# Kernel tuning notes

Measured on AMD Instinct MI355X. Metric: run time of the kernel, lower is better.

The kernel has to match this reference:

```python
import jax, jax.numpy as jnp
import numpy as np
import math

WIN = (2, 7, 7)      # (wd, wh, ww) 3D window
SHIFT = (1, 3, 3)    # cyclic shift per dim
HEADS = 4
DIM = 128
MLP_HIDDEN = 4 * DIM


def _layernorm(x, w, b, eps=1e-5):
    m = x.mean(-1, keepdims=True)
    v = jnp.var(x, axis=-1, keepdims=True)
    return (x - m) * jax.lax.rsqrt(v + eps) * w + b


def setup_inputs() -> dict:
    key = jax.random.key(0)
    ks = jax.random.split(key, 6)
    C, H = DIM, MLP_HIDDEN
    p = lambda k, shape: jax.random.normal(k, shape, jnp.float32) * 0.02
    return {
        "x": jax.random.normal(ks[0], (4, 8, 56, 56, C), jnp.float32),
        "norm1_w": jnp.ones((C,), jnp.float32),
        "norm1_b": jnp.zeros((C,), jnp.float32),
        "qkv_w": p(ks[1], (C, 3 * C)),
        "qkv_b": jnp.zeros((3 * C,), jnp.float32),
        "proj_w": p(ks[2], (C, C)),
        "proj_b": jnp.zeros((C,), jnp.float32),
        "norm2_w": jnp.ones((C,), jnp.float32),
        "norm2_b": jnp.zeros((C,), jnp.float32),
        "fc1_w": p(ks[3], (C, H)),
        "fc1_b": jnp.zeros((H,), jnp.float32),
        "fc2_w": p(ks[4], (H, C)),
        "fc2_b": jnp.zeros((C,), jnp.float32),
    }


def reference(x, norm1_w, norm1_b, qkv_w, qkv_b, proj_w, proj_b,
              norm2_w, norm2_b, fc1_w, fc1_b, fc2_w, fc2_b):
    B, D, H, W, C = x.shape
    wd, wh, ww = WIN
    sd, sh, sw = SHIFT
    nd, nh, nw = D // wd, H // wh, W // ww
    N = wd * wh * ww          # tokens per window (98)
    hd = C // HEADS
    scale = 1.0 / math.sqrt(hd)

    # ---- part1: norm1 -> cyclic shift -> window partition -> MHA -> reverse ----
    h = _layernorm(x, norm1_w, norm1_b)
    h = jnp.roll(h, (-sd, -sh, -sw), axis=(1, 2, 3))
    # window partition: (B,D,H,W,C) -> (B*nWindows, N, C)
    xw = h.reshape(B, nd, wd, nh, wh, nw, ww, C)
    xw = xw.transpose(0, 1, 3, 5, 2, 4, 6, 7).reshape(-1, N, C)

    qkv = (xw @ qkv_w + qkv_b).reshape(-1, N, 3, HEADS, hd).transpose(2, 0, 3, 1, 4)
    q, k, v = qkv[0], qkv[1], qkv[2]      # each (Bw, heads, N, hd)
    scores = jnp.einsum('bhnc,bhmc->bhnm', q, k) * scale
    attn = jax.nn.softmax(scores, axis=-1)
    out = jnp.einsum('bhnm,bhmc->bhnc', attn, v)
    out = out.transpose(0, 2, 1, 3).reshape(-1, N, C)
    out = out @ proj_w + proj_b

    # window reverse: (B*nWindows, N, C) -> (B,D,H,W,C)
    out = out.reshape(B, nd, nh, nw, wd, wh, ww, C)
    out = out.transpose(0, 1, 4, 2, 5, 3, 6, 7).reshape(B, D, H, W, C)
    out = jnp.roll(out, (sd, sh, sw), axis=(1, 2, 3))

    x = x + out  # residual (drop_path = identity)

    # ---- part2: norm2 -> MLP (Linear -> SiLU -> Linear) -> residual ----
    h2 = _layernorm(x, norm2_w, norm2_b)
    h2 = jax.nn.silu(h2 @ fc1_w + fc1_b) @ fc2_w + fc2_b
    return x + h2
```

## Files before the change

### kernel.cpp

```cpp
#include <hip/hip_runtime.h>

typedef unsigned short u16;
typedef unsigned int u32;
typedef __bf16 bf16x8 __attribute__((ext_vector_type(8)));
typedef float f32x4 __attribute__((ext_vector_type(4)));
typedef u16 u16x8 __attribute__((ext_vector_type(8)));
typedef u16 u16x2 __attribute__((ext_vector_type(2)));

__device__ __forceinline__ float bf2f(u16 u) {
    union { u32 u; float f; } c; c.u = ((u32)u) << 16; return c.f;
}
__device__ __forceinline__ u16 f2bf(float f) {
    union { float f; u32 u; } c; c.f = f;
    u32 r = c.u + 0x7fffu + ((c.u >> 16) & 1u);
    return (u16)(r >> 16);
}
__device__ __forceinline__ u16 f2bfn(float f) {
    union { __bf16 h; u16 u; } c; c.h = (__bf16)f; return c.u;
}
__device__ __forceinline__ bf16x8 ld_frag(const u16* p) {
    return *reinterpret_cast<const bf16x8*>(p);
}

__global__ __launch_bounds__(256) void k_wT(
    const float* __restrict__ qkv_w, const float* __restrict__ proj_w,
    const float* __restrict__ fc1_w, const float* __restrict__ fc2_w,
    u16* __restrict__ qkvT, u16* __restrict__ projT,
    u16* __restrict__ fc1T, u16* __restrict__ fc2T)
{
    int t = blockIdx.x * 256 + threadIdx.x;
    if (t < 49152) { int k = t / 384, n = t % 384; qkvT[n*128 + k] = f2bf(qkv_w[t]); }
    if (t < 16384) { int k = t / 128, n = t % 128; projT[n*128 + k] = f2bf(proj_w[t]); }
    if (t < 65536) { int k = t / 512, n = t % 512; fc1T[n*128 + k] = f2bf(fc1_w[t]); }
    if (t < 65536) { int k = t / 128, n = t % 128; fc2T[n*512 + k] = f2bf(fc2_w[t]); }
}

__global__ __launch_bounds__(256) void k_ln1_part(
    const float* __restrict__ x, const float* __restrict__ w, const float* __restrict__ b,
    u16* __restrict__ xw)
{
    int wv = threadIdx.x >> 6, l = threadIdx.x & 63;
    int g = blockIdx.x * 4 + wv;
    int wi = g / 98, n = g % 98;
    int iw = wi & 7, ih = (wi >> 3) & 7, id = (wi >> 6) & 3, bb = wi >> 8;
    int tw = n % 7, tt = n / 7, th = tt % 7, td = tt / 7;
    int d  = (id * 2 + td + 1) & 7;
    int hh = ih * 7 + th + 3; if (hh >= 56) hh -= 56;
    int ww = iw * 7 + tw + 3; if (ww >= 56) ww -= 56;
    long src = ((((long)bb * 8 + d) * 56 + hh) * 56 + ww) * 128;
    float2 v = *(const float2*)(x + src + l * 2);
    float f0 = v.x, f1 = v.y;
    float s = f0 + f1, s2 = f0*f0 + f1*f1;
    #pragma unroll
    for (int o = 32; o; o >>= 1) { s += __shfl_xor(s, o); s2 += __shfl_xor(s2, o); }
    float mean = s * (1.f/128.f);
    float var  = s2 * (1.f/128.f) - mean*mean;
    float rstd = rsqrtf(var + 1e-5f);
    float y0 = (f0 - mean) * rstd * w[l*2]   + b[l*2];
    float y1 = (f1 - mean) * rstd * w[l*2+1] + b[l*2+1];
    u16x2 o2; o2[0] = f2bf(y0); o2[1] = f2bf(y1);
    *(u16x2*)(xw + (long)g * 128 + l * 2) = o2;
}

__global__ __launch_bounds__(256) void k_gemm128(
    const u16* __restrict__ A, const u16* __restrict__ BT,
    const float* __restrict__ bias, u16* __restrict__ out, int ldo)
{
    __shared__ __align__(16) u16 la[128*136];
    __shared__ __align__(16) u16 lb[128*136];
    int m0 = blockIdx.x * 128, n0 = blockIdx.y * 128;
    int t = threadIdx.x;
    #pragma unroll
    for (int i = 0; i < 8; i++) {
        int u = t + i * 256;
        int r = u >> 4, c = u & 15;
        *(u16x8*)&la[r*136 + c*8] = *(const u16x8*)&A [(long)(m0 + r)*128 + c*8];
        *(u16x8*)&lb[r*136 + c*8] = *(const u16x8*)&BT[(long)(n0 + r)*128 + c*8];
    }
    __syncthreads();
    int wv = t >> 6, l = t & 63;
    int wm = (wv & 1) * 64, wn = (wv >> 1) * 64;
    int lr = l & 15, lk = (l >> 4) * 8;
    f32x4 acc[4][4] = {};
    #pragma unroll
    for (int kk = 0; kk < 4; kk++) {
        bf16x8 af[4], bfr[4];
        #pragma unroll
        for (int mi = 0; mi < 4; mi++) af[mi]  = ld_frag(&la[(wm + mi*16 + lr)*136 + kk*32 + lk]);
        #pragma unroll
        for (int ni = 0; ni < 4; ni++) bfr[ni] = ld_frag(&lb[(wn + ni*16 + lr)*136 + kk*32 + lk]);
        #pragma unroll
        for (int mi = 0; mi < 4; mi++)
            #pragma unroll
            for (int ni = 0; ni < 4; ni++)
                acc[mi][ni] = __builtin_amdgcn_mfma_f32_16x16x32_bf16(af[mi], bfr[ni], acc[mi][ni], 0, 0, 0);
    }
    int rb = (l >> 4) * 4;
    #pragma unroll
    for (int mi = 0; mi < 4; mi++)
        #pragma unroll
        for (int ni = 0; ni < 4; ni++) {
            int col = n0 + wn + ni*16 + lr;
            float bv = bias[col];
            #pragma unroll
            for (int r = 0; r < 4; r++) {
                int row = m0 + wm + mi*16 + rb + r;
                out[(long)row*ldo + col] = f2bf(acc[mi][ni][r] + bv);
            }
        }
}

__global__ __launch_bounds__(256) void k_attn(
    const u16* __restrict__ qkv, u16* __restrict__ attn_out)
{
    __shared__ __align__(16) u16 lq[128*40];
    __shared__ __align__(16) u16 lk[128*40];
    __shared__ __align__(16) u16 lvt[32*136];
    __shared__ __align__(16) u16 lp[4][16*136];
    int wi = blockIdx.x, h = blockIdx.y;
    int t = threadIdx.x;
    int wv = t >> 6, l = t & 63;
    const long base = (long)wi * 98 * 384 + h * 32;
    u16* lpw = lp[wv];
    {
        u16x8 z8 = {};
        for (int i = l; i < 272; i += 64) *(u16x8*)&lpw[i*8] = z8;
    }
    #pragma unroll
    for (int i = 0; i < 4; i++) {
        int u = t + i * 256;
        int mat = u >> 9, row = (u >> 2) & 127, ch = u & 3;
        u16x8 v = {};
        if (row < 98) v = *(const u16x8*)&qkv[base + (long)row*384 + mat*128 + ch*8];
        u16* dst = mat ? lk : lq;
        *(u16x8*)&dst[row*40 + ch*8] = v;
    }
    #pragma unroll
    for (int i = 0; i < 2; i++) {
        int u = t + i * 256;
        int row = u >> 2, ch = u & 3;
        u16x8 v = {};
        if (row < 98) v = *(const u16x8*)&qkv[base + (long)row*384 + 256 + ch*8];
        #pragma unroll
        for (int j = 0; j < 8; j++) lvt[(ch*8 + j)*136 + row] = v[j];
    }
    __syncthreads();
    int lr = l & 15, lg = l >> 4, lkk = lg * 8;
    const float scale = 0.17677669529663687f;
    for (int rt = wv; rt < 7; rt += 4) {
        bf16x8 qa = ld_frag(&lq[(rt*16 + lr)*40 + lkk]);
        f32x4 s[7];
        #pragma unroll
        for (int ct = 0; ct < 7; ct++) {
            bf16x8 kb = ld_frag(&lk[(ct*16 + lr)*40 + lkk]);
            f32x4 zz = {0.f, 0.f, 0.f, 0.f};
            s[ct] = __builtin_amdgcn_mfma_f32_16x16x32_bf16(qa, kb, zz, 0, 0, 0);
        }
        #pragma unroll
        for (int ct = 0; ct < 7; ct++) {
            bool valid = (ct < 6) || (lr < 2);
            #pragma unroll
            for (int r = 0; r < 4; r++)
                s[ct][r] = valid ? s[ct][r] * scale : -1e30f;
        }
        f32x4 mx;
        #pragma unroll
        for (int r = 0; r < 4; r++) {
            float m = s[0][r];
            #pragma unroll
            for (int ct = 1; ct < 7; ct++) m = fmaxf(m, s[ct][r]);
            #pragma unroll
            for (int o = 1; o < 16; o <<= 1) m = fmaxf(m, __shfl_xor(m, o));
            mx[r] = m;
        }
        f32x4 sum = {0.f, 0.f, 0.f, 0.f};
        #pragma unroll
        for (int ct = 0; ct < 7; ct++)
            #pragma unroll
            for (int r = 0; r < 4; r++) {
                s[ct][r] = __expf(s[ct][r] - mx[r]);
                sum[r] += s[ct][r];
            }
        #pragma unroll
        for (int r = 0; r < 4; r++) {
            float ss = sum[r];
            #pragma unroll
            for (int o = 1; o < 16; o <<= 1) ss += __shfl_xor(ss, o);
            sum[r] = 1.f / ss;
        }
        #pragma unroll
        for (int ct = 0; ct < 7; ct++)
            #pragma unroll
            for (int r = 0; r < 4; r++)
                lpw[(lg*4 + r)*136 + ct*16 + lr] = f2bf(s[ct][r] * sum[r]);
        #pragma unroll
        for (int ni = 0; ni < 2; ni++) {
            f32x4 acc = {0.f, 0.f, 0.f, 0.f};
            #pragma unroll
            for (int kk = 0; kk < 4; kk++) {
                bf16x8 pa = ld_frag(&lpw[lr*136 + kk*32 + lkk]);
                bf16x8 vb = ld_frag(&lvt[(ni*16 + lr)*136 + kk*32 + lkk]);
                acc = __builtin_amdgcn_mfma_f32_16x16x32_bf16(pa, vb, acc, 0, 0, 0);
            }
            #pragma unroll
            for (int r = 0; r < 4; r++) {
                int row = rt*16 + lg*4 + r;
                if (row < 98)
                    attn_out[((long)wi*98 + row)*128 + h*32 + ni*16 + lr] = f2bf(acc[r]);
            }
        }
    }
}

__global__ __launch_bounds__(256, 4) void k_mlp2(
    const u16* __restrict__ pout, const float* __restrict__ x,
    const float* __restrict__ w2, const float* __restrict__ b2n,
    const u16* __restrict__ fc1T, const float* __restrict__ b1,
    const u16* __restrict__ fc2T, const float* __restrict__ b2,
    u16* __restrict__ x1g, float* __restrict__ out)
{
    __shared__ __align__(16) u16 lh [64*136];
    __shared__ __align__(16) u16 lhc[2][64*72];
    int m0 = blockIdx.x * 64;
    int t = threadIdx.x;
    int wv = t >> 6, l = t & 63;
    int lr = l & 15, lg = l >> 4, lk = lg * 8;
    {
        float4 w2a = *(const float4*)&w2 [lr*8];
        float4 w2b = *(const float4*)&w2 [lr*8 + 4];
        float4 b2a = *(const float4*)&b2n[lr*8];
        float4 b2b = *(const float4*)&b2n[lr*8 + 4];
        float w2v[8] = {w2a.x,w2a.y,w2a.z,w2a.w,w2b.x,w2b.y,w2b.z,w2b.w};
        float b2v[8] = {b2a.x,b2a.y,b2a.z,b2a.w,b2b.x,b2b.y,b2b.z,b2b.w};
        for (int it = 0; it < 4; it++) {
            int row = wv*16 + it*4 + lg;
            int g = m0 + row;
            int ww = g % 56; int t1 = g / 56;
            int hh = t1 % 56; int t2 = t1 / 56;
            int d = t2 & 7, bb = t2 >> 3;
            int d2 = (d + 7) & 7;
            int hs = hh - 3; if (hs < 0) hs += 56;
            int ws_ = ww - 3; if (ws_ < 0) ws_ += 56;
            int id = d2 >> 1, td = d2 & 1;
            int ih = hs / 7, th = hs % 7;
            int iw = ws_ / 7, tw = ws_ % 7;
            int wi = ((bb*4 + id)*8 + ih)*8 + iw;
            int n  = (td*7 + th)*7 + tw;
            long prow = ((long)wi*98 + n) * 128;
            u16x8 pv = *(const u16x8*)&pout[prow + lr*8];
            float4 xa = *(const float4*)&x[(long)g*128 + lr*8];
            float4 xb = *(const float4*)&x[(long)g*128 + lr*8 + 4];
            float v[8];
            v[0] = bf2f(pv[0]) + xa.x; v[1] = bf2f(pv[1]) + xa.y;
            v[2] = bf2f(pv[2]) + xa.z; v[3] = bf2f(pv[3]) + xa.w;
            v[4] = bf2f(pv[4]) + xb.x; v[5] = bf2f(pv[5]) + xb.y;
            v[6] = bf2f(pv[6]) + xb.z; v[7] = bf2f(pv[7]) + xb.w;
            float s = 0.f, s2 = 0.f;
            #pragma unroll
            for (int j = 0; j < 8; j++) { s += v[j]; s2 += v[j]*v[j]; }
            #pragma unroll
            for (int o = 1; o < 16; o <<= 1) { s += __shfl_xor(s, o); s2 += __shfl_xor(s2, o); }
            float mean = s * (1.f/128.f), var = s2 * (1.f/128.f) - mean*mean;
            float rstd = rsqrtf(var + 1e-5f);
            u16x8 xo, ho;
            #pragma unroll
            for (int j = 0; j < 8; j++) {
                xo[j] = f2bfn(v[j]);
                ho[j] = f2bfn((v[j] - mean)*rstd*w2v[j] + b2v[j]);
            }
            *(u16x8*)&x1g[(long)g*128 + lr*8] = xo;
            *(u16x8*)&lh [row*136 + lr*8] = ho;
        }
    }
    __syncthreads();
    f32x4 oacc[4][2] = {};
    for (int ch = 0; ch < 8; ch++) {
        char* lc = (char*)lhc[ch & 1];
        int un0 = ch*64 + wv*16;
        bf16x8 bfr[4];
        #pragma unroll
        for (int kk = 0; kk < 4; kk++)
            bfr[kk] = ld_frag(&fc1T[(un0 + lr)*128 + kk*32 + lk]);
        float bv = b1[un0 + lr];
        #pragma unroll
        for (int mt = 0; mt < 4; mt++) {
            f32x4 acc = {0.f, 0.f, 0.f, 0.f};
            #pragma unroll
            for (int kk = 0; kk < 4; kk++) {
                bf16x8 a = ld_frag(&lh[(mt*16 + lr)*136 + kk*32 + lk]);
                acc = __builtin_amdgcn_mfma_f32_16x16x32_bf16(a, bfr[kk], acc, 0, 0, 0);
            }
            #pragma unroll
            for (int r = 0; r < 4; r++) {
                int row = mt*16 + lg*4 + r;
                float vv = acc[r] + bv;
                vv = __fdividef(vv, 1.f + __expf(-vv));
                int byo = row*144 + ((((wv*16 + lr)*2)) ^ ((row & 8) << 2));
                *(u16*)(lc + byo) = f2bfn(vv);
            }
        }
        __syncthreads();
        #pragma unroll
        for (int nt = 0; nt < 2; nt++) {
            int col = wv*32 + nt*16 + lr;
            bf16x8 b0 = ld_frag(&fc2T[(long)col*512 + ch*64 + lk]);
            bf16x8 b1f = ld_frag(&fc2T[(long)col*512 + ch*64 + 32 + lk]);
            #pragma unroll
            for (int mt = 0; mt < 4; mt++) {
                int rr = mt*16 + lr;
                int xw_ = (rr & 8) << 2;
                bf16x8 a0 = *(const bf16x8*)(lc + rr*144 + ((lg*16)      ^ xw_));
                bf16x8 a1 = *(const bf16x8*)(lc + rr*144 + ((lg*16 + 64) ^ xw_));
                oacc[mt][nt] = __builtin_amdgcn_mfma_f32_16x16x32_bf16(a0, b0, oacc[mt][nt], 0, 0, 0);
                oacc[mt][nt] = __builtin_amdgcn_mfma_f32_16x16x32_bf16(a1, b1f, oacc[mt][nt], 0, 0, 0);
            }
        }
    }
    #pragma unroll
    for (int nt = 0; nt < 2; nt++) {
        int col = wv*32 + nt*16 + lr;
        float bv = b2[col];
        #pragma unroll
        for (int mt = 0; mt < 4; mt++) {
            #pragma unroll
            for (int r = 0; r < 4; r++) {
                int row = mt*16 + lg*4 + r;
                out[(long)(m0 + row)*128 + col] =
                    oacc[mt][nt][r] + bv + bf2f(x1g[(long)(m0 + row)*128 + col]);
            }
        }
    }
}

extern "C" void kernel_launch(void* const* d_in, const int* in_sizes, int n_in,
                              void* d_out, int out_size, void* d_ws, size_t ws_size,
                              hipStream_t stream)
{
    const float* x      = (const float*)d_in[0];
    const float* n1w    = (const float*)d_in[1];
    const float* n1b    = (const float*)d_in[2];
    const float* qkv_w  = (const float*)d_in[3];
    const float* qkv_b  = (const float*)d_in[4];
    const float* proj_w = (const float*)d_in[5];
    const float* proj_b = (const float*)d_in[6];
    const float* n2w    = (const float*)d_in[7];
    const float* n2b    = (const float*)d_in[8];
    const float* fc1_w  = (const float*)d_in[9];
    const float* fc1_b  = (const float*)d_in[10];
    const float* fc2_w  = (const float*)d_in[11];
    const float* fc2_b  = (const float*)d_in[12];
    float* out = (float*)d_out;

    u16* ws16  = (u16*)d_ws;
    u16* xw    = ws16;
    u16* qkv   = xw + 12845056;
    u16* qkvT  = qkv + 38535168;
    u16* projT = qkvT + 49152;
    u16* fc1T  = projT + 16384;
    u16* fc2T  = fc1T + 65536;

    k_wT<<<256, 256, 0, stream>>>(qkv_w, proj_w, fc1_w, fc2_w, qkvT, projT, fc1T, fc2T);
    k_ln1_part<<<25088, 256, 0, stream>>>(x, n1w, n1b, xw);
    dim3 gq(784, 3);
    k_gemm128<<<gq, 256, 0, stream>>>(xw, qkvT, qkv_b, qkv, 384);
    dim3 ga(1024, 4);
    k_attn<<<ga, 256, 0, stream>>>(qkv, xw);
    dim3 gp(784, 1);
    k_gemm128<<<gp, 256, 0, stream>>>(xw, projT, proj_b, qkv, 128);
    k_mlp2<<<1568, 256, 0, stream>>>(qkv , x, n2w, n2b,
                                     fc1T, fc1_b, fc2T, fc2_b,
                                     xw , out);
}
```

Measured before the change: 192.1 us.

## Fuse LayerNorm1, shift and window partition into QKV GEMM kernel

Replaces the separate LN1 and window-partition kernel plus the QKV GEMM with one kernel. Each block normalizes its 128 gathered tokens directly into shared memory, then loops over the three 128-column output chunks of the QKV weights. This removes the bf16 round trip of the normalized activations through global memory and one launch. The cost is that the grid drops from 784x3 to 784 blocks, each doing three GEMM tiles serially, which lowers parallelism.

```diff
diff --git a/kernel.cpp b/kernel.cpp
--- a/kernel.cpp
+++ b/kernel.cpp
@@ -35,31 +35,88 @@
     if (t < 65536) { int k = t / 128, n = t % 128; fc2T[n*512 + k] = f2bf(fc2_w[t]); }
 }
 
-__global__ __launch_bounds__(256) void k_ln1_part(
-    const float* __restrict__ x, const float* __restrict__ w, const float* __restrict__ b,
-    u16* __restrict__ xw)
-{
-    int wv = threadIdx.x >> 6, l = threadIdx.x & 63;
-    int g = blockIdx.x * 4 + wv;
-    int wi = g / 98, n = g % 98;
-    int iw = wi & 7, ih = (wi >> 3) & 7, id = (wi >> 6) & 3, bb = wi >> 8;
-    int tw = n % 7, tt = n / 7, th = tt % 7, td = tt / 7;
-    int d  = (id * 2 + td + 1) & 7;
-    int hh = ih * 7 + th + 3; if (hh >= 56) hh -= 56;
-    int ww = iw * 7 + tw + 3; if (ww >= 56) ww -= 56;
-    long src = ((((long)bb * 8 + d) * 56 + hh) * 56 + ww) * 128;
-    float2 v = *(const float2*)(x + src + l * 2);
-    float f0 = v.x, f1 = v.y;
-    float s = f0 + f1, s2 = f0*f0 + f1*f1;
-    #pragma unroll
-    for (int o = 32; o; o >>= 1) { s += __shfl_xor(s, o); s2 += __shfl_xor(s2, o); }
-    float mean = s * (1.f/128.f);
-    float var  = s2 * (1.f/128.f) - mean*mean;
-    float rstd = rsqrtf(var + 1e-5f);
-    float y0 = (f0 - mean) * rstd * w[l*2]   + b[l*2];
-    float y1 = (f1 - mean) * rstd * w[l*2+1] + b[l*2+1];
-    u16x2 o2; o2[0] = f2bf(y0); o2[1] = f2bf(y1);
-    *(u16x2*)(xw + (long)g * 128 + l * 2) = o2;
+__global__ __launch_bounds__(256) void k_qkv(
+    const float* __restrict__ x, const float* __restrict__ w1, const float* __restrict__ b1n,
+    const u16* __restrict__ qkvT, const float* __restrict__ qkv_b,
+    u16* __restrict__ out)
+{
+    __shared__ __align__(16) u16 la[128*136];
+    __shared__ __align__(16) u16 lb[128*136];
+    int m0 = blockIdx.x * 128;
+    int t = threadIdx.x;
+    int wv = t >> 6, l = t & 63;
+    int lr = l & 15, lk = (l >> 4) * 8;
+    {
+        int c = t & 15;
+        float4 wa = *(const float4*)&w1 [c*8], wb = *(const float4*)&w1 [c*8 + 4];
+        float4 ba = *(const float4*)&b1n[c*8], bbv = *(const float4*)&b1n[c*8 + 4];
+        float w1v[8] = {wa.x,wa.y,wa.z,wa.w,wb.x,wb.y,wb.z,wb.w};
+        float b1v[8] = {ba.x,ba.y,ba.z,ba.w,bbv.x,bbv.y,bbv.z,bbv.w};
+        #pragma unroll
+        for (int i = 0; i < 8; i++) {
+            int r = (t >> 4) + i*16;
+            int g = m0 + r;
+            int wi = g / 98, n = g % 98;
+            int iw = wi & 7, ih = (wi >> 3) & 7, id = (wi >> 6) & 3, bb = wi >> 8;
+            int tw = n % 7, tt = n / 7, th = tt % 7, td = tt / 7;
+            int d  = (id * 2 + td + 1) & 7;
+            int hh = ih * 7 + th + 3; if (hh >= 56) hh -= 56;
+            int ww = iw * 7 + tw + 3; if (ww >= 56) ww -= 56;
+            long src = ((((long)bb * 8 + d) * 56 + hh) * 56 + ww) * 128;
+            float4 xa = *(const float4*)&x[src + c*8];
+            float4 xb = *(const float4*)&x[src + c*8 + 4];
+            float v[8] = {xa.x,xa.y,xa.z,xa.w,xb.x,xb.y,xb.z,xb.w};
+            float s = 0.f, s2 = 0.f;
+            #pragma unroll
+            for (int j = 0; j < 8; j++) { s += v[j]; s2 += v[j]*v[j]; }
+            #pragma unroll
+            for (int o = 1; o < 16; o <<= 1) { s += __shfl_xor(s, o); s2 += __shfl_xor(s2, o); }
+            float mean = s * (1.f/128.f), var = s2 * (1.f/128.f) - mean*mean;
+            float rstd = rsqrtf(var + 1e-5f);
+            u16x8 ho;
+            #pragma unroll
+            for (int j = 0; j < 8; j++)
+                ho[j] = f2bfn((v[j] - mean)*rstd*w1v[j] + b1v[j]);
+            *(u16x8*)&la[r*136 + c*8] = ho;
+        }
+    }
+    for (int nc = 0; nc < 3; nc++) {
+        __syncthreads();
+        #pragma unroll
+        for (int i = 0; i < 8; i++) {
+            int r = (t >> 4) + i*16, c = t & 15;
+            *(u16x8*)&lb[r*136 + c*8] = *(const u16x8*)&qkvT[(long)(nc*128 + r)*128 + c*8];
+        }
+        __syncthreads();
+        int wm = (wv & 1) * 64, wn = (wv >> 1) * 64;
+        f32x4 acc[4][4] = {};
+        #pragma unroll
+        for (int kk = 0; kk < 4; kk++) {
+            bf16x8 af[4], bfr[4];
+            #pragma unroll
+            for (int mi = 0; mi < 4; mi++) af[mi]  = ld_frag(&la[(wm + mi*16 + lr)*136 + kk*32 + lk]);
+            #pragma unroll
+            for (int ni = 0; ni < 4; ni++) bfr[ni] = ld_frag(&lb[(wn + ni*16 + lr)*136 + kk*32 + lk]);
+            #pragma unroll
+            for (int mi = 0; mi < 4; mi++)
+                #pragma unroll
+                for (int ni = 0; ni < 4; ni++)
+                    acc[mi][ni] = __builtin_amdgcn_mfma_f32_16x16x32_bf16(af[mi], bfr[ni], acc[mi][ni], 0, 0, 0);
+        }
+        int rb = (l >> 4) * 4;
+        #pragma unroll
+        for (int mi = 0; mi < 4; mi++)
+            #pragma unroll
+            for (int ni = 0; ni < 4; ni++) {
+                int col = nc*128 + wn + ni*16 + lr;
+                float bv = qkv_b[col];
+                #pragma unroll
+                for (int r = 0; r < 4; r++) {
+                    int row = m0 + wm + mi*16 + rb + r;
+                    out[(long)row*384 + col] = f2bf(acc[mi][ni][r] + bv);
+                }
+            }
+    }
 }
 
 __global__ __launch_bounds__(256) void k_gemm128(
@@ -360,9 +417,7 @@
     u16* fc2T  = fc1T + 65536;
 
     k_wT<<<256, 256, 0, stream>>>(qkv_w, proj_w, fc1_w, fc2_w, qkvT, projT, fc1T, fc2T);
-    k_ln1_part<<<25088, 256, 0, stream>>>(x, n1w, n1b, xw);
-    dim3 gq(784, 3);
-    k_gemm128<<<gq, 256, 0, stream>>>(xw, qkvT, qkv_b, qkv, 384);
+    k_qkv<<<784, 256, 0, stream>>>(x, n1w, n1b, qkvT, qkv_b, qkv);
     dim3 ga(1024, 4);
     k_attn<<<ga, 256, 0, stream>>>(qkv, xw);
     dim3 gp(784, 1);
```

After: 195.1 us. Within noise of the previous version (+1.5%).
